# Performance work log

Measured on AMD Instinct MI355X. Metric: run time of the kernel, lower is better.

## Reference

```python
import jax, jax.numpy as jnp
import numpy as np

BITS = 8
EPS = 0.01  # eps in max_scale_rounded_power
QMAX = float(1 << (BITS - 1))  # 128.0; quantize multiplies by (1<<bits)/scale=2 -> 2^(bits-1)


def _max_scale_rounded_power(x, axis):
    # max_scale: clamp(max(|x|, axis), min=eps); then round scale up to a power of 2
    m = jnp.maximum(jnp.max(jnp.abs(x), axis=axis), EPS)
    return jnp.exp2(jnp.ceil(jnp.log2(m)))


def _dmd_dequant(x):
    """quantize_dmd_alternating(iters=2) followed by recreate_from_dmd.

    x: (..., R, C). i=0 scales columns (reduce over rows, dim=-2),
    i=1 scales rows (reduce over cols, dim=-1). quantize(x,0,2,bits) =
    clamp(round(x * 2^(bits-1)), -2^(bits-1), 2^(bits-1)-1), and the row
    scale is divided by 2^(bits-1) before reconstruction.
    """
    s_col = _max_scale_rounded_power(x, -2)          # (..., C)
    x = x / s_col[..., None, :]
    s_row = _max_scale_rounded_power(x, -1)          # (..., R)
    x = x / s_row[..., :, None]
    q = jnp.clip(jnp.round(x * QMAX), -QMAX, QMAX - 1.0)
    # recreate_from_dmd(s_col, q, s_row / 2^(bits-1))
    return s_col[..., None, :] * q * (s_row / QMAX)[..., :, None]


def setup_inputs() -> dict:
    key = jax.random.key(0)
    k1, k2, k3 = jax.random.split(key, 3)
    B, S, NX, NF = 8, 4096, 1024, 1024
    x = jax.random.normal(k1, (B, S, NX), dtype=jnp.float32)
    weight = jax.random.normal(k2, (NX, NF), dtype=jnp.float32) * 0.02
    bias = jax.random.normal(k3, (NF,), dtype=jnp.float32) * 0.01
    return {"x": x, "weight": weight, "bias": bias}


def reference(x, weight, bias):
    B, S, nx = x.shape
    nf = weight.shape[-1]
    xq = _dmd_dequant(x.reshape(-1, nx))   # (B*S, nx) dequantized
    yq = _dmd_dequant(weight)              # (nx, nf) dequantized
    out = xq @ yq + bias                   # (B*S, nf)
    return out.reshape(B, S, nf)
```

## Files before the change

### kernel.cpp

```cpp
#include <hip/hip_runtime.h>
#include <hip/hip_bf16.h>
#include <stdint.h>

#define NXK 1024
#define NFN 1024
#define EPSQ 0.01f

typedef __bf16 bf16x8 __attribute__((ext_vector_type(8)));
typedef float f32x4 __attribute__((ext_vector_type(4)));

#define AS1(p) ((const __attribute__((address_space(1))) void*)(p))
#define AS3(p) ((__attribute__((address_space(3))) void*)(p))

__device__ __forceinline__ float p2ceil(float m) {
    unsigned u = __float_as_uint(m);
    if ((u & 0x7fffffu) == 0) return m;
    return __uint_as_float((((u >> 23) & 0xffu) + 1u) << 23);
}

__device__ __forceinline__ unsigned short f2bf(float f) {
    __bf16 h = (__bf16)f;
    return __builtin_bit_cast(unsigned short, h);
}

#define RPB 32
__global__ __launch_bounds__(256) void colmax_part_kernel(const float* __restrict__ X,
                                                          float* __restrict__ pmax) {
    const int t = threadIdx.x;
    const size_t r0 = (size_t)blockIdx.x * RPB;
    const float4* Xv = (const float4*)X;
    float m0 = 0.f, m1 = 0.f, m2 = 0.f, m3 = 0.f;
#pragma unroll 8
    for (int i = 0; i < RPB; ++i) {
        float4 v = Xv[(r0 + i) * (NXK / 4) + t];
        m0 = fmaxf(m0, fabsf(v.x));
        m1 = fmaxf(m1, fabsf(v.y));
        m2 = fmaxf(m2, fabsf(v.z));
        m3 = fmaxf(m3, fabsf(v.w));
    }
    float4 o; o.x = m0; o.y = m1; o.z = m2; o.w = m3;
    ((float4*)(pmax + (size_t)blockIdx.x * NXK))[t] = o;
}

__global__ __launch_bounds__(256) void colmax_reduce_kernel(const float* __restrict__ pmax,
                                                            int npart,
                                                            float* __restrict__ cscale) {
    __shared__ float red[8][32];
    const int t = threadIdx.x;
    const int c = blockIdx.x * 32 + (t & 31);
    const int chunk = t >> 5;
    const int per = npart >> 3;
    float m = 0.f;
    for (int r = chunk * per; r < (chunk + 1) * per; ++r)
        m = fmaxf(m, pmax[(size_t)r * NXK + c]);
    red[chunk][t & 31] = m;
    __syncthreads();
    if (t < 32) {
        float v = red[0][t];
#pragma unroll
        for (int i = 1; i < 8; ++i) v = fmaxf(v, red[i][t]);
        cscale[blockIdx.x * 32 + t] = p2ceil(fmaxf(v, EPSQ));
    }
}

__global__ __launch_bounds__(256) void colmax_atomic_kernel(const float* __restrict__ X,
                                                            unsigned int* __restrict__ cmax) {
    const int t = threadIdx.x;
    const size_t r0 = (size_t)blockIdx.x * RPB;
    const float4* Xv = (const float4*)X;
    float m0 = 0.f, m1 = 0.f, m2 = 0.f, m3 = 0.f;
#pragma unroll 8
    for (int i = 0; i < RPB; ++i) {
        float4 v = Xv[(r0 + i) * (NXK / 4) + t];
        m0 = fmaxf(m0, fabsf(v.x));
        m1 = fmaxf(m1, fabsf(v.y));
        m2 = fmaxf(m2, fabsf(v.z));
        m3 = fmaxf(m3, fabsf(v.w));
    }
    atomicMax(&cmax[4 * t + 0], __float_as_uint(m0));
    atomicMax(&cmax[4 * t + 1], __float_as_uint(m1));
    atomicMax(&cmax[4 * t + 2], __float_as_uint(m2));
    atomicMax(&cmax[4 * t + 3], __float_as_uint(m3));
}

template <int TRANSPOSE, int PRESCALED>
__global__ __launch_bounds__(256) void rowquant_kernel(const float* __restrict__ X,
                                                       const void* __restrict__ colinfo,
                                                       unsigned short* __restrict__ Q) {
    const int wave = threadIdx.x >> 6, lane = threadIdx.x & 63;
    const int m = blockIdx.x * 4 + wave;
    const float4* Xr = (const float4*)(X + (size_t)m * NXK);

    float r[16], sc[16];
    float amax = 0.f;
#pragma unroll
    for (int c = 0; c < 4; ++c) {
        const float4 v = Xr[lane + 64 * c];
        if (PRESCALED) {
            const float4 s = ((const float4*)colinfo)[lane + 64 * c];
            sc[4 * c + 0] = s.x; sc[4 * c + 1] = s.y;
            sc[4 * c + 2] = s.z; sc[4 * c + 3] = s.w;
        } else {
            const uint4 cb = ((const uint4*)colinfo)[lane + 64 * c];
            sc[4 * c + 0] = p2ceil(fmaxf(__uint_as_float(cb.x), EPSQ));
            sc[4 * c + 1] = p2ceil(fmaxf(__uint_as_float(cb.y), EPSQ));
            sc[4 * c + 2] = p2ceil(fmaxf(__uint_as_float(cb.z), EPSQ));
            sc[4 * c + 3] = p2ceil(fmaxf(__uint_as_float(cb.w), EPSQ));
        }
        r[4 * c + 0] = v.x / sc[4 * c + 0];
        r[4 * c + 1] = v.y / sc[4 * c + 1];
        r[4 * c + 2] = v.z / sc[4 * c + 2];
        r[4 * c + 3] = v.w / sc[4 * c + 3];
        amax = fmaxf(amax, fmaxf(fmaxf(fabsf(r[4 * c + 0]), fabsf(r[4 * c + 1])),
                                 fmaxf(fabsf(r[4 * c + 2]), fabsf(r[4 * c + 3]))));
    }
#pragma unroll
    for (int s = 1; s < 64; s <<= 1) amax = fmaxf(amax, __shfl_xor(amax, s, 64));

    const float srow = p2ceil(fmaxf(amax, EPSQ));
    const float inv = 128.0f / srow;
    const float rs = srow * 0.0078125f;
#pragma unroll
    for (int c = 0; c < 4; ++c) {
        const float q0 = fminf(fmaxf(rintf(r[4 * c + 0] * inv), -128.0f), 127.0f);
        const float q1 = fminf(fmaxf(rintf(r[4 * c + 1] * inv), -128.0f), 127.0f);
        const float q2 = fminf(fmaxf(rintf(r[4 * c + 2] * inv), -128.0f), 127.0f);
        const float q3 = fminf(fmaxf(rintf(r[4 * c + 3] * inv), -128.0f), 127.0f);
        if (TRANSPOSE) {
            Q[(size_t)(4 * (lane + 64 * c) + 0) * NXK + m] = f2bf(q0 * (sc[4 * c + 0] * rs));
            Q[(size_t)(4 * (lane + 64 * c) + 1) * NXK + m] = f2bf(q1 * (sc[4 * c + 1] * rs));
            Q[(size_t)(4 * (lane + 64 * c) + 2) * NXK + m] = f2bf(q2 * (sc[4 * c + 2] * rs));
            Q[(size_t)(4 * (lane + 64 * c) + 3) * NXK + m] = f2bf(q3 * (sc[4 * c + 3] * rs));
        } else {
            ushort4 o;
            o.x = f2bf(q0 * (sc[4 * c + 0] * rs));
            o.y = f2bf(q1 * (sc[4 * c + 1] * rs));
            o.z = f2bf(q2 * (sc[4 * c + 2] * rs));
            o.w = f2bf(q3 * (sc[4 * c + 3] * rs));
            ((ushort4*)(Q + (size_t)m * NXK))[lane + 64 * c] = o;
        }
    }
}

#define GX (NFN / 128)
__global__ __launch_bounds__(256) void gemm_kernel(const unsigned short* __restrict__ A,
                                                   const unsigned short* __restrict__ BT,
                                                   const float* __restrict__ bias,
                                                   float* __restrict__ C, int M) {
    constexpr int K = NXK, N = NFN;
    __shared__ unsigned short As[128][32];
    __shared__ unsigned short Bs[128][32];

    const int tid = threadIdx.x;
    const int wave = tid >> 6, lane = tid & 63;
    const int wr = wave >> 1, wc = wave & 1;

    const int nwg = GX * (M / 128);
    int lin = blockIdx.y * GX + blockIdx.x;
    {
        const int q = nwg >> 3, r = nwg & 7;
        const int xcd = lin & 7, idx = lin >> 3;
        lin = (xcd < r ? xcd * (q + 1) : r * (q + 1) + (xcd - r) * q) + idx;
    }
    const int bm = (lin / GX) * 128, bn = (lin % GX) * 128;

    f32x4 acc[4][4] = {};

    const int strow = wave * 32 + (lane >> 2);
    const int stcol = (lane & 3) * 8;
    const unsigned short* gA = A + (size_t)(bm + strow) * K + stcol;
    const unsigned short* gB = BT + (size_t)(bn + strow) * K + stcol;
    unsigned short* lA0 = &As[wave * 32][0];
    unsigned short* lA1 = &As[wave * 32 + 16][0];
    unsigned short* lB0 = &Bs[wave * 32][0];
    unsigned short* lB1 = &Bs[wave * 32 + 16][0];

    for (int k0 = 0; k0 < K; k0 += 32) {
        __builtin_amdgcn_global_load_lds(AS1(gA + k0),          AS3(lA0), 16, 0, 0);
        __builtin_amdgcn_global_load_lds(AS1(gA + 16 * K + k0), AS3(lA1), 16, 0, 0);
        __builtin_amdgcn_global_load_lds(AS1(gB + k0),          AS3(lB0), 16, 0, 0);
        __builtin_amdgcn_global_load_lds(AS1(gB + 16 * K + k0), AS3(lB1), 16, 0, 0);
        asm volatile("s_waitcnt vmcnt(0)" ::: "memory");
        __syncthreads();

        bf16x8 af[4], bf[4];
#pragma unroll
        for (int i = 0; i < 4; ++i) {
            af[i] = *(const bf16x8*)&As[wr * 64 + i * 16 + (lane & 15)][(lane >> 4) * 8];
            bf[i] = *(const bf16x8*)&Bs[wc * 64 + i * 16 + (lane & 15)][(lane >> 4) * 8];
        }
#pragma unroll
        for (int mi = 0; mi < 4; ++mi)
#pragma unroll
            for (int ni = 0; ni < 4; ++ni)
                acc[mi][ni] = __builtin_amdgcn_mfma_f32_16x16x32_bf16(af[mi], bf[ni], acc[mi][ni], 0, 0, 0);
        __syncthreads();
    }

#pragma unroll
    for (int mi = 0; mi < 4; ++mi) {
#pragma unroll
        for (int ni = 0; ni < 4; ++ni) {
            const int col = bn + wc * 64 + ni * 16 + (lane & 15);
            const float bv = bias[col];
#pragma unroll
            for (int j = 0; j < 4; ++j) {
                const int row = bm + wr * 64 + mi * 16 + (lane >> 4) * 4 + j;
                C[(size_t)row * N + col] = acc[mi][ni][j] + bv;
            }
        }
    }
}

extern "C" void kernel_launch(void* const* d_in, const int* in_sizes, int n_in,
                              void* d_out, int out_size, void* d_ws, size_t ws_size,
                              hipStream_t stream) {
    const float* x    = (const float*)d_in[0];
    const float* w    = (const float*)d_in[1];
    const float* bias = (const float*)d_in[2];
    float* out = (float*)d_out;
    const int M = in_sizes[0] / NXK;
    const int NPART = M / RPB;

    char* ws = (char*)d_ws;
    unsigned short* xq = (unsigned short*)ws;
    size_t off = (size_t)M * NXK * sizeof(unsigned short);
    unsigned short* wqT = (unsigned short*)(ws + off);
    off += (size_t)NFN * NXK * sizeof(unsigned short);
    float* pmax = (float*)(ws + off);
    off += (size_t)NPART * NXK * sizeof(float);
    float* cscale = (float*)(ws + off);
    off += NXK * sizeof(float);
    unsigned int* cmw = (unsigned int*)(ws + off);

    hipMemsetAsync(cmw, 0, NFN * sizeof(unsigned int), stream);

    colmax_part_kernel<<<NPART, 256, 0, stream>>>(x, pmax);
    colmax_atomic_kernel<<<NXK / RPB, 256, 0, stream>>>(w, cmw);
    colmax_reduce_kernel<<<NXK / 32, 256, 0, stream>>>(pmax, NPART, cscale);
    rowquant_kernel<0, 1><<<M / 4, 256, 0, stream>>>(x, cscale, xq);
    rowquant_kernel<1, 0><<<NXK / 4, 256, 0, stream>>>(w, cmw, wqT);
    gemm_kernel<<<dim3(GX, M / 128), 256, 0, stream>>>(xq, wqT, bias, out, M);
}
```

Before: 382.6 us.

## Replace GEMM with 256x256 tile, 8-wave pipelined kernel with swizzled LDS

Replaces the 128x128, BK=32 GEMM with a 256x256 tile, BK=64 kernel using 8 waves and 128KB of dynamic LDS split into four half-tile slots. Global-to-LDS loads for later k-steps are issued between MFMA quarters, with partial vmcnt waits, so loads overlap compute. An XOR swizzle is meant to avoid LDS bank conflicts. This aims to raise MFMA utilization and data reuse, at the cost of higher register and LDS use, which limits occupancy.

Measured after the change: 362.4 us. 1.06x faster.

```diff
diff --git a/kernel.cpp b/kernel.cpp
--- a/kernel.cpp
+++ b/kernel.cpp
@@ -142,74 +142,147 @@
     }
 }
 
-#define GX (NFN / 128)
-__global__ __launch_bounds__(256) void gemm_kernel(const unsigned short* __restrict__ A,
-                                                   const unsigned short* __restrict__ BT,
-                                                   const float* __restrict__ bias,
-                                                   float* __restrict__ C, int M) {
-    constexpr int K = NXK, N = NFN;
-    __shared__ unsigned short As[128][32];
-    __shared__ unsigned short Bs[128][32];
+#define BM 256
+#define BN 256
+#define BKT 64
+#define NT (NXK / BKT)
+#define GXT (NFN / BN)
+
+#define BARRIER() do { asm volatile("" ::: "memory"); __builtin_amdgcn_s_barrier(); asm volatile("" ::: "memory"); } while (0)
+#define WAIT_LGKM0() do { asm volatile("s_waitcnt lgkmcnt(0)" ::: "memory"); __builtin_amdgcn_sched_barrier(0); } while (0)
+#define WAIT_VM(n) do { asm volatile("s_waitcnt vmcnt(" #n ")" ::: "memory"); __builtin_amdgcn_sched_barrier(0); } while (0)
+
+__device__ __forceinline__ void stage_half(const unsigned short* __restrict__ G,
+                                           int gr0, int k0, char* ldsbase, int tid) {
+#pragma unroll
+    for (int i = 0; i < 2; ++i) {
+        const int chunk = i * 512 + tid;
+        const int r = chunk >> 3;
+        const int cb = (chunk & 7) * 16;
+        const int scb = cb ^ ((r & 7) << 4);
+        const char* src = (const char*)(G + (size_t)(gr0 + r) * NXK + k0) + scb;
+        char* dst = ldsbase + (size_t)(i * 512 + (tid & ~63)) * 16;
+        __builtin_amdgcn_global_load_lds(AS1(src), AS3(dst), 16, 0, 0);
+    }
+}
+
+__global__ __launch_bounds__(512, 2) void gemm8_kernel(const unsigned short* __restrict__ A,
+                                                       const unsigned short* __restrict__ BT,
+                                                       const float* __restrict__ bias,
+                                                       float* __restrict__ C, int M) {
+    extern __shared__ char smem[];
+    char* Alds = smem;
+    char* Blds = smem + 65536;
 
     const int tid = threadIdx.x;
-    const int wave = tid >> 6, lane = tid & 63;
-    const int wr = wave >> 1, wc = wave & 1;
-
-    const int nwg = GX * (M / 128);
-    int lin = blockIdx.y * GX + blockIdx.x;
+    const int wv = tid >> 6, lane = tid & 63;
+    const int wm = wv >> 2, wn = wv & 3;
+
+    const int nwg = (M / BM) * GXT;
+    int lin = blockIdx.x;
     {
-        const int q = nwg >> 3, r = nwg & 7;
-        const int xcd = lin & 7, idx = lin >> 3;
-        lin = (xcd < r ? xcd * (q + 1) : r * (q + 1) + (xcd - r) * q) + idx;
-    }
-    const int bm = (lin / GX) * 128, bn = (lin % GX) * 128;
-
-    f32x4 acc[4][4] = {};
-
-    const int strow = wave * 32 + (lane >> 2);
-    const int stcol = (lane & 3) * 8;
-    const unsigned short* gA = A + (size_t)(bm + strow) * K + stcol;
-    const unsigned short* gB = BT + (size_t)(bn + strow) * K + stcol;
-    unsigned short* lA0 = &As[wave * 32][0];
-    unsigned short* lA1 = &As[wave * 32 + 16][0];
-    unsigned short* lB0 = &Bs[wave * 32][0];
-    unsigned short* lB1 = &Bs[wave * 32 + 16][0];
-
-    for (int k0 = 0; k0 < K; k0 += 32) {
-        __builtin_amdgcn_global_load_lds(AS1(gA + k0),          AS3(lA0), 16, 0, 0);
-        __builtin_amdgcn_global_load_lds(AS1(gA + 16 * K + k0), AS3(lA1), 16, 0, 0);
-        __builtin_amdgcn_global_load_lds(AS1(gB + k0),          AS3(lB0), 16, 0, 0);
-        __builtin_amdgcn_global_load_lds(AS1(gB + 16 * K + k0), AS3(lB1), 16, 0, 0);
-        asm volatile("s_waitcnt vmcnt(0)" ::: "memory");
-        __syncthreads();
-
-        bf16x8 af[4], bf[4];
-#pragma unroll
-        for (int i = 0; i < 4; ++i) {
-            af[i] = *(const bf16x8*)&As[wr * 64 + i * 16 + (lane & 15)][(lane >> 4) * 8];
-            bf[i] = *(const bf16x8*)&Bs[wc * 64 + i * 16 + (lane & 15)][(lane >> 4) * 8];
+        const int q = nwg >> 3;
+        lin = (lin & 7) * q + (lin >> 3);
+    }
+    const int bm = (lin >> 2) * BM;
+    const int bn = (lin & 3) * BN;
+
+    float bv[4];
+#pragma unroll
+    for (int nf = 0; nf < 4; ++nf) bv[nf] = bias[bn + wn * 64 + nf * 16 + (lane & 15)];
+    asm volatile("" : "+v"(bv[0]), "+v"(bv[1]), "+v"(bv[2]), "+v"(bv[3]));
+    asm volatile("s_waitcnt vmcnt(0)" ::: "memory");
+
+    f32x4 acc[8][4] = {};
+    bf16x8 a[4][2], b[2][2][2];
+
+    const int xr = (lane & 7) << 4;
+    const int colx0 = ((lane >> 4) * 16) ^ xr;
+    const int colx1 = (((lane >> 4) * 16) + 64) ^ xr;
+    const int arow = lane & 15;
+    const int brow0 = (wn & 1) * 64 + (lane & 15);
+
+#define LOAD_A(mh) do { _Pragma("unroll") for (int mf = 0; mf < 4; ++mf) { \
+        const int lr = (mh) * 64 + mf * 16 + arow; \
+        a[mf][0] = *(const bf16x8*)(Asl + lr * 128 + colx0); \
+        a[mf][1] = *(const bf16x8*)(Asl + lr * 128 + colx1); } } while (0)
+
+#define LOAD_B(nh) do { _Pragma("unroll") for (int nf = 0; nf < 2; ++nf) { \
+        const int lr = brow0 + (nh) * 32 + nf * 16; \
+        b[nh][nf][0] = *(const bf16x8*)(Bsl + lr * 128 + colx0); \
+        b[nh][nf][1] = *(const bf16x8*)(Bsl + lr * 128 + colx1); } } while (0)
+
+#define MFMA_Q(mh, nh) do { \
+        __builtin_amdgcn_s_setprio(1); \
+        _Pragma("unroll") for (int mf = 0; mf < 4; ++mf) \
+        _Pragma("unroll") for (int nf = 0; nf < 2; ++nf) { \
+            acc[(mh)*4+mf][(nh)*2+nf] = __builtin_amdgcn_mfma_f32_16x16x32_bf16(a[mf][0], b[nh][nf][0], acc[(mh)*4+mf][(nh)*2+nf], 0, 0, 0); \
+            acc[(mh)*4+mf][(nh)*2+nf] = __builtin_amdgcn_mfma_f32_16x16x32_bf16(a[mf][1], b[nh][nf][1], acc[(mh)*4+mf][(nh)*2+nf], 0, 0, 0); } \
+        __builtin_amdgcn_s_setprio(0); \
+        __builtin_amdgcn_sched_barrier(0); } while (0)
+
+    stage_half(A,  bm,       0,   Alds + 0 * 16384, tid);
+    stage_half(BT, bn,       0,   Blds + 0 * 16384, tid);
+    stage_half(A,  bm + 128, 0,   Alds + 1 * 16384, tid);
+    stage_half(BT, bn + 128, 0,   Blds + 1 * 16384, tid);
+    stage_half(A,  bm,       BKT, Alds + 2 * 16384, tid);
+    stage_half(BT, bn,       BKT, Blds + 2 * 16384, tid);
+    WAIT_VM(4);
+    BARRIER();
+
+    for (int t = 0; t < NT; ++t) {
+        const int sN1 = (2 * t + 3) & 3;
+        const int sT0 = (2 * t) & 3;
+        const char* Asl = Alds + (size_t)(((2 * t) + wm) & 3) * 16384;
+        const char* Bsl = Blds + (size_t)(((2 * t) + (wn >> 1)) & 3) * 16384;
+        const int k0n = (t + 1) * BKT, k0nn = (t + 2) * BKT;
+        const bool p1 = (t + 1) < NT, p2 = (t + 2) < NT;
+
+        LOAD_A(0);
+        LOAD_B(0);
+        if (p1) stage_half(A, bm + 128, k0n, Alds + sN1 * 16384, tid);
+        BARRIER();
+        WAIT_LGKM0();
+        MFMA_Q(0, 0);
+        BARRIER();
+
+        LOAD_B(1);
+        if (p1) stage_half(BT, bn + 128, k0n, Blds + sN1 * 16384, tid);
+        BARRIER();
+        WAIT_LGKM0();
+        MFMA_Q(0, 1);
+        BARRIER();
+
+        LOAD_A(1);
+        if (p2) stage_half(BT, bn, k0nn, Blds + sT0 * 16384, tid);
+        BARRIER();
+        WAIT_LGKM0();
+        MFMA_Q(1, 0);
+        BARRIER();
+
+        if (p2) stage_half(A, bm, k0nn, Alds + sT0 * 16384, tid);
+        BARRIER();
+        WAIT_LGKM0();
+        MFMA_Q(1, 1);
+        if (p2) { WAIT_VM(4); }
+        else if (p1) { WAIT_VM(0); }
+        BARRIER();
+    }
+
+#pragma unroll
+    for (int mf8 = 0; mf8 < 8; ++mf8) {
+#pragma unroll
+        for (int nf = 0; nf < 4; ++nf) {
+            const int col = bn + wn * 64 + nf * 16 + (lane & 15);
+            const size_t rb = (size_t)(bm + wm * 128 + mf8 * 16 + (lane >> 4) * 4) * NFN + col;
+#pragma unroll
+            for (int j = 0; j < 4; ++j)
+                C[rb + (size_t)j * NFN] = acc[mf8][nf][j] + bv[nf];
         }
-#pragma unroll
-        for (int mi = 0; mi < 4; ++mi)
-#pragma unroll
-            for (int ni = 0; ni < 4; ++ni)
-                acc[mi][ni] = __builtin_amdgcn_mfma_f32_16x16x32_bf16(af[mi], bf[ni], acc[mi][ni], 0, 0, 0);
-        __syncthreads();
-    }
-
-#pragma unroll
-    for (int mi = 0; mi < 4; ++mi) {
-#pragma unroll
-        for (int ni = 0; ni < 4; ++ni) {
-            const int col = bn + wc * 64 + ni * 16 + (lane & 15);
-            const float bv = bias[col];
-#pragma unroll
-            for (int j = 0; j < 4; ++j) {
-                const int row = bm + wr * 64 + mi * 16 + (lane >> 4) * 4 + j;
-                C[(size_t)row * N + col] = acc[mi][ni][j] + bv;
-            }
-        }
-    }
+    }
+#undef LOAD_A
+#undef LOAD_B
+#undef MFMA_Q
 }
 
 extern "C" void kernel_launch(void* const* d_in, const int* in_sizes, int n_in,
@@ -233,6 +306,9 @@
     off += NXK * sizeof(float);
     unsigned int* cmw = (unsigned int*)(ws + off);
 
+    hipFuncSetAttribute((const void*)gemm8_kernel,
+                        hipFuncAttributeMaxDynamicSharedMemorySize, 131072);
+
     hipMemsetAsync(cmw, 0, NFN * sizeof(unsigned int), stream);
 
     colmax_part_kernel<<<NPART, 256, 0, stream>>>(x, pmax);
@@ -240,5 +316,7 @@
     colmax_reduce_kernel<<<NXK / 32, 256, 0, stream>>>(pmax, NPART, cscale);
     rowquant_kernel<0, 1><<<M / 4, 256, 0, stream>>>(x, cscale, xq);
     rowquant_kernel<1, 0><<<NXK / 4, 256, 0, stream>>>(w, cmw, wqT);
-    gemm_kernel<<<dim3(GX, M / 128), 256, 0, stream>>>(xq, wqT, bias, out, M);
-}
+
+    const int nwg = (M / BM) * GXT;
+    gemm8_kernel<<<nwg, 512, 131072, stream>>>(xq, wqT, bias, out, M);
+}
```
